# Optimization experiments

Hardware: AMD Instinct MI355X
Metric: run time of the kernel (lower is better)

The kernel has to match this reference:

```python
import jax, jax.numpy as jnp
import numpy as np

N, D, F_NUM = 262144, 128, 64
TEMPERATURE = 0.5
EPS = 1e-8  # torch F.cosine_similarity eps


def setup_inputs() -> dict:
    key = jax.random.key(0)
    k1, k2 = jax.random.split(key)
    embeddings = jax.random.normal(k1, (N, D), dtype=jnp.float32)
    families = jax.random.randint(k2, (N,), 0, F_NUM, dtype=jnp.int32)
    return {"embeddings": embeddings, "families": families}


def reference(embeddings, families):
    T = TEMPERATURE
    n = embeddings.shape[0]
    # Per-family prototype means (segment mean). All F_NUM families are
    # present w.h.p.; guard counts with max(.,1) to avoid div-by-zero.
    ones = jnp.ones((n,), dtype=embeddings.dtype)
    counts = jax.ops.segment_sum(ones, families, num_segments=F_NUM)
    sums = jax.ops.segment_sum(embeddings, families, num_segments=F_NUM)
    protos = sums / jnp.maximum(counts, 1.0)[:, None]  # [F, D]

    # Cosine similarity matrix [N, F], matching torch eps semantics:
    # x.y / max(||x|| * ||y||, eps)
    dots = embeddings @ protos.T                              # [N, F]
    e_norm = jnp.linalg.norm(embeddings, axis=1)              # [N]
    p_norm = jnp.linalg.norm(protos, axis=1)                  # [F]
    sim = dots / jnp.maximum(e_norm[:, None] * p_norm[None, :], EPS)

    pos = jnp.take_along_axis(sim, families[:, None].astype(jnp.int32), axis=1)[:, 0]  # [N]
    # Source quirk: logits already divided by T, then divided by T again
    # inside logsumexp -> effective sim / T^2. The concatenated logits
    # contain pos + all other prototypes = all F prototypes exactly once.
    lse = jax.nn.logsumexp(sim / (T * T), axis=1)             # [N]
    per_sample = -pos / T + lse                               # [N]
    loss = jnp.sum(per_sample) / n
    return loss[None]  # torch returns shape (1,)
```

## Files before the change

### kernel.cpp

```cpp
#include <hip/hip_runtime.h>
#include <math.h>


#define D_DIM 128
#define F_NUM 64
#define ROWS_A 512

typedef __attribute__((ext_vector_type(8))) short short8;
typedef __attribute__((ext_vector_type(4))) float f32x4;

static __device__ __forceinline__ unsigned short f2bf(float x) {
  union { float f; unsigned u; } v; v.f = x;
  unsigned r = v.u + 0x7FFFu + ((v.u >> 16) & 1u);
  return (unsigned short)(r >> 16);
}

__global__ __launch_bounds__(256, 2) void pass_a(
    const float* __restrict__ emb, const int* __restrict__ fam,
    float* __restrict__ psum)
{
  int t = threadIdx.x, w = t >> 6, lane = t & 63;
  int m16 = lane & 15, q = lane >> 4;
  int dimBase = w * 32;

  f32x4 acc[4][2] = {};
  int rb0 = blockIdx.x * ROWS_A;

  #pragma unroll 2
  for (int s = 0; s < ROWS_A / 32; ++s) {
    int rb = rb0 + s * 32;
    const int* fp = fam + rb + q * 8;
    int fj[8];
    #pragma unroll
    for (int j = 0; j < 8; ++j) fj[j] = fp[j];

    const float* eb = emb + (size_t)(rb + q * 8) * D_DIM + dimBase + m16;
    float x0[8], x1[8];
    #pragma unroll
    for (int j = 0; j < 8; ++j) {
      x0[j] = eb[j * D_DIM];
      x1[j] = eb[j * D_DIM + 16];
    }

    short8 af[4];
    #pragma unroll
    for (int ft = 0; ft < 4; ++ft)
      #pragma unroll
      for (int j = 0; j < 8; ++j)
        af[ft][j] = (fj[j] == ft * 16 + m16) ? (short)0x3F80 : (short)0;

    short8 h0, l0, h1, l1;
    #pragma unroll
    for (int j = 0; j < 8; ++j) {
      unsigned b0 = __float_as_uint(x0[j]);
      h0[j] = (short)(b0 >> 16);
      l0[j] = (short)f2bf(x0[j] - __uint_as_float(b0 & 0xFFFF0000u));
      unsigned b1 = __float_as_uint(x1[j]);
      h1[j] = (short)(b1 >> 16);
      l1[j] = (short)f2bf(x1[j] - __uint_as_float(b1 & 0xFFFF0000u));
    }

    #pragma unroll
    for (int ft = 0; ft < 4; ++ft) {
      acc[ft][0] = __builtin_amdgcn_mfma_f32_16x16x32_bf16(af[ft], h0, acc[ft][0], 0, 0, 0);
      acc[ft][0] = __builtin_amdgcn_mfma_f32_16x16x32_bf16(af[ft], l0, acc[ft][0], 0, 0, 0);
      acc[ft][1] = __builtin_amdgcn_mfma_f32_16x16x32_bf16(af[ft], h1, acc[ft][1], 0, 0, 0);
      acc[ft][1] = __builtin_amdgcn_mfma_f32_16x16x32_bf16(af[ft], l1, acc[ft][1], 0, 0, 0);
    }
  }

  float* outp = psum + (size_t)blockIdx.x * (F_NUM * D_DIM) + dimBase + m16;
  #pragma unroll
  for (int ft = 0; ft < 4; ++ft)
    #pragma unroll
    for (int i = 0; i < 4; ++i) {
      int f = ft * 16 + q * 4 + i;
      outp[(size_t)f * D_DIM]      = acc[ft][0][i];
      outp[(size_t)f * D_DIM + 16] = acc[ft][1][i];
    }
}

__global__ __launch_bounds__(256) void pass_b(
    const float* __restrict__ psum, unsigned short* __restrict__ protoB,
    int nPart)
{
  __shared__ float4 sh[256];
  int t = threadIdx.x, f = blockIdx.x;
  int d4 = t & 31, pg = t >> 5;
  const float4* p4 = (const float4*)psum;
  float4 s = make_float4(0.f, 0.f, 0.f, 0.f);
  int per = nPart >> 3;
  #pragma unroll 8
  for (int i = 0; i < per; ++i) {
    float4 a = p4[(size_t)(pg + 8 * i) * (F_NUM * D_DIM / 4) + f * 32 + d4];
    s.x += a.x; s.y += a.y; s.z += a.z; s.w += a.w;
  }
  sh[t] = s;
  __syncthreads();
  if (t < 32) {
    float4 rsum = sh[t];
    #pragma unroll
    for (int g = 1; g < 8; ++g) {
      float4 a = sh[g * 32 + t];
      rsum.x += a.x; rsum.y += a.y; rsum.z += a.z; rsum.w += a.w;
    }
    float n2 = rsum.x * rsum.x + rsum.y * rsum.y +
               rsum.z * rsum.z + rsum.w * rsum.w;
    n2 += __shfl_xor(n2, 1);  n2 += __shfl_xor(n2, 2);  n2 += __shfl_xor(n2, 4);
    n2 += __shfl_xor(n2, 8);  n2 += __shfl_xor(n2, 16);
    float inv = rsqrtf(fmaxf(n2, 1e-24f));
    ushort4 u;
    u.x = f2bf(rsum.x * inv); u.y = f2bf(rsum.y * inv);
    u.z = f2bf(rsum.z * inv); u.w = f2bf(rsum.w * inv);
    ((ushort4*)protoB)[f * 32 + t] = u;
  }
}

__global__ __launch_bounds__(256) void pass_c(
    const float* __restrict__ emb, const int* __restrict__ fam,
    const unsigned short* __restrict__ protoB, float* __restrict__ part)
{
  __shared__ float sWp[4];
  int t = threadIdx.x, w = t >> 6, lane = t & 63;
  int m16 = lane & 15, q = lane >> 4;
  int S0 = blockIdx.x * 128 + w * 32;

  const float4* E4 = (const float4*)emb;
  const short8* P8 = (const short8*)protoB;

  size_t e0 = (size_t)(S0 + m16) * 32 + q * 2;
  size_t e1 = e0 + 16 * 32;
  int pb = m16 * 16 + q;

  f32x4 acc[2][4] = {};
  float s2a = 0.f, s2b = 0.f;

  #pragma unroll
  for (int ks = 0; ks < 4; ++ks) {
    short8 a0 = P8[pb + ks * 4];
    short8 a1 = P8[pb + 256 + ks * 4];
    short8 a2 = P8[pb + 512 + ks * 4];
    short8 a3 = P8[pb + 768 + ks * 4];

    float4 va = E4[e0 + ks * 8], vb = E4[e0 + ks * 8 + 1];
    s2a += va.x * va.x + va.y * va.y + va.z * va.z + va.w * va.w +
           vb.x * vb.x + vb.y * vb.y + vb.z * vb.z + vb.w * vb.w;
    short8 b0;
    b0[0] = (short)f2bf(va.x); b0[1] = (short)f2bf(va.y);
    b0[2] = (short)f2bf(va.z); b0[3] = (short)f2bf(va.w);
    b0[4] = (short)f2bf(vb.x); b0[5] = (short)f2bf(vb.y);
    b0[6] = (short)f2bf(vb.z); b0[7] = (short)f2bf(vb.w);
    acc[0][0] = __builtin_amdgcn_mfma_f32_16x16x32_bf16(a0, b0, acc[0][0], 0, 0, 0);
    acc[0][1] = __builtin_amdgcn_mfma_f32_16x16x32_bf16(a1, b0, acc[0][1], 0, 0, 0);
    acc[0][2] = __builtin_amdgcn_mfma_f32_16x16x32_bf16(a2, b0, acc[0][2], 0, 0, 0);
    acc[0][3] = __builtin_amdgcn_mfma_f32_16x16x32_bf16(a3, b0, acc[0][3], 0, 0, 0);

    float4 vc = E4[e1 + ks * 8], vd = E4[e1 + ks * 8 + 1];
    s2b += vc.x * vc.x + vc.y * vc.y + vc.z * vc.z + vc.w * vc.w +
           vd.x * vd.x + vd.y * vd.y + vd.z * vd.z + vd.w * vd.w;
    short8 b1;
    b1[0] = (short)f2bf(vc.x); b1[1] = (short)f2bf(vc.y);
    b1[2] = (short)f2bf(vc.z); b1[3] = (short)f2bf(vc.w);
    b1[4] = (short)f2bf(vd.x); b1[5] = (short)f2bf(vd.y);
    b1[6] = (short)f2bf(vd.z); b1[7] = (short)f2bf(vd.w);
    acc[1][0] = __builtin_amdgcn_mfma_f32_16x16x32_bf16(a0, b1, acc[1][0], 0, 0, 0);
    acc[1][1] = __builtin_amdgcn_mfma_f32_16x16x32_bf16(a1, b1, acc[1][1], 0, 0, 0);
    acc[1][2] = __builtin_amdgcn_mfma_f32_16x16x32_bf16(a2, b1, acc[1][2], 0, 0, 0);
    acc[1][3] = __builtin_amdgcn_mfma_f32_16x16x32_bf16(a3, b1, acc[1][3], 0, 0, 0);
  }

  s2a += __shfl_xor(s2a, 16); s2a += __shfl_xor(s2a, 32);
  s2b += __shfl_xor(s2b, 16); s2b += __shfl_xor(s2b, 32);
  float rn0 = rsqrtf(fmaxf(s2a, 1e-20f));
  float rn1 = rsqrtf(fmaxf(s2b, 1e-20f));
  int fr0 = fam[S0 + m16], fr1 = fam[S0 + 16 + m16];

  float wp = 0.f;
  {
    int fh = fr0 >> 4, fq = (fr0 >> 2) & 3, fl = fr0 & 3;
    float es = 0.f, ps = 0.f;
    #pragma unroll
    for (int ft = 0; ft < 4; ++ft)
      #pragma unroll
      for (int i = 0; i < 4; ++i) {
        float sim = acc[0][ft][i] * rn0;
        es += __expf(4.f * sim - 4.f);
        ps += (fq == q && fh == ft && fl == i) ? sim : 0.f;
      }
    es += __shfl_xor(es, 16); es += __shfl_xor(es, 32);
    ps += __shfl_xor(ps, 16); ps += __shfl_xor(ps, 32);
    if (q == 0) wp += 4.f + __logf(es) - 2.f * ps;
  }
  {
    int fh = fr1 >> 4, fq = (fr1 >> 2) & 3, fl = fr1 & 3;
    float es = 0.f, ps = 0.f;
    #pragma unroll
    for (int ft = 0; ft < 4; ++ft)
      #pragma unroll
      for (int i = 0; i < 4; ++i) {
        float sim = acc[1][ft][i] * rn1;
        es += __expf(4.f * sim - 4.f);
        ps += (fq == q && fh == ft && fl == i) ? sim : 0.f;
      }
    es += __shfl_xor(es, 16); es += __shfl_xor(es, 32);
    ps += __shfl_xor(ps, 16); ps += __shfl_xor(ps, 32);
    if (q == 0) wp += 4.f + __logf(es) - 2.f * ps;
  }

  wp += __shfl_xor(wp, 1);  wp += __shfl_xor(wp, 2);  wp += __shfl_xor(wp, 4);
  wp += __shfl_xor(wp, 8);  wp += __shfl_xor(wp, 16); wp += __shfl_xor(wp, 32);
  if (lane == 0) sWp[w] = wp;
  __syncthreads();
  if (t == 0) part[blockIdx.x] = sWp[0] + sWp[1] + sWp[2] + sWp[3];
}

__global__ __launch_bounds__(256) void pass_d(
    const float* __restrict__ part, float* __restrict__ out, float invN, int n)
{
  __shared__ float red[4];
  int t = threadIdx.x, w = t >> 6, lane = t & 63;
  float s = 0.f;
  for (int i = t; i < n; i += 256) s += part[i];
  s += __shfl_xor(s, 1);  s += __shfl_xor(s, 2);  s += __shfl_xor(s, 4);
  s += __shfl_xor(s, 8);  s += __shfl_xor(s, 16); s += __shfl_xor(s, 32);
  if (lane == 0) red[w] = s;
  __syncthreads();
  if (t == 0) out[0] = (red[0] + red[1] + red[2] + red[3]) * invN;
}

extern "C" void kernel_launch(void* const* d_in, const int* in_sizes, int n_in,
                              void* d_out, int out_size, void* d_ws, size_t ws_size,
                              hipStream_t stream) {
  const float* emb = (const float*)d_in[0];
  const int* fam = (const int*)d_in[1];
  int N = in_sizes[0] / D_DIM;
  int blocksA = N / ROWS_A;
  int blocksC = N / 128;

  float* ws = (float*)d_ws;
  float* psum = ws;
  size_t off = (size_t)blocksA * (F_NUM * D_DIM);
  unsigned short* protoB = (unsigned short*)(ws + off); off += (F_NUM * D_DIM) / 2;
  float* part = ws + off;

  pass_a<<<blocksA, 256, 0, stream>>>(emb, fam, psum);
  pass_b<<<F_NUM, 256, 0, stream>>>(psum, protoB, blocksA);
  pass_c<<<blocksC, 256, 0, stream>>>(emb, fam, protoB, part);
  pass_d<<<1, 256, 0, stream>>>(part, (float*)d_out, 1.0f / (float)N, blocksC);
}
```

Baseline: 235.2 us.

## Halve pass_a rows, pack bf16 operands, widen pass_b, fuse final reduction via atomics

Halves the rows per pass_a block and raises its occupancy hint. It also builds the bf16 hi/lo split and one-hot operands as packed 32-bit words, with the low part truncated instead of rounded. pass_b now uses 1024 threads to reduce the larger number of partials and zeroes the output. pass_c atomically adds its scaled partial into the output, which removes the pass_d launch. The intent is more parallelism in pass_a, fewer conversion instructions and one fewer launch, at the cost of more partial-sum traffic, a float result order that varies between runs, and slightly lower precision from truncation.

```diff
diff --git a/kernel.cpp b/kernel.cpp
--- a/kernel.cpp
+++ b/kernel.cpp
@@ -4,10 +4,11 @@
 
 #define D_DIM 128
 #define F_NUM 64
-#define ROWS_A 512
+#define ROWS_A 256
 
 typedef __attribute__((ext_vector_type(8))) short short8;
 typedef __attribute__((ext_vector_type(4))) float f32x4;
+typedef union { short8 s; unsigned u[4]; } pack8;
 
 static __device__ __forceinline__ unsigned short f2bf(float x) {
   union { float f; unsigned u; } v; v.f = x;
@@ -15,7 +16,7 @@
   return (unsigned short)(r >> 16);
 }
 
-__global__ __launch_bounds__(256, 2) void pass_a(
+__global__ __launch_bounds__(256, 4) void pass_a(
     const float* __restrict__ emb, const int* __restrict__ fam,
     float* __restrict__ psum)
 {
@@ -42,30 +43,39 @@
       x1[j] = eb[j * D_DIM + 16];
     }
 
-    short8 af[4];
-    #pragma unroll
-    for (int ft = 0; ft < 4; ++ft)
+    pack8 H0, L0, H1, L1;
+    #pragma unroll
+    for (int p = 0; p < 4; ++p) {
+      unsigned a0 = __float_as_uint(x0[2 * p]);
+      unsigned a1 = __float_as_uint(x0[2 * p + 1]);
+      H0.u[p] = (a0 >> 16) | (a1 & 0xFFFF0000u);
+      float la = x0[2 * p]     - __uint_as_float(a0 & 0xFFFF0000u);
+      float lb = x0[2 * p + 1] - __uint_as_float(a1 & 0xFFFF0000u);
+      L0.u[p] = (__float_as_uint(la) >> 16) | (__float_as_uint(lb) & 0xFFFF0000u);
+      unsigned b0 = __float_as_uint(x1[2 * p]);
+      unsigned b1 = __float_as_uint(x1[2 * p + 1]);
+      H1.u[p] = (b0 >> 16) | (b1 & 0xFFFF0000u);
+      float lc = x1[2 * p]     - __uint_as_float(b0 & 0xFFFF0000u);
+      float ld = x1[2 * p + 1] - __uint_as_float(b1 & 0xFFFF0000u);
+      L1.u[p] = (__float_as_uint(lc) >> 16) | (__float_as_uint(ld) & 0xFFFF0000u);
+    }
+
+    pack8 AF[4];
+    #pragma unroll
+    for (int ft = 0; ft < 4; ++ft) {
+      int tgt = ft * 16 + m16;
       #pragma unroll
-      for (int j = 0; j < 8; ++j)
-        af[ft][j] = (fj[j] == ft * 16 + m16) ? (short)0x3F80 : (short)0;
-
-    short8 h0, l0, h1, l1;
-    #pragma unroll
-    for (int j = 0; j < 8; ++j) {
-      unsigned b0 = __float_as_uint(x0[j]);
-      h0[j] = (short)(b0 >> 16);
-      l0[j] = (short)f2bf(x0[j] - __uint_as_float(b0 & 0xFFFF0000u));
-      unsigned b1 = __float_as_uint(x1[j]);
-      h1[j] = (short)(b1 >> 16);
-      l1[j] = (short)f2bf(x1[j] - __uint_as_float(b1 & 0xFFFF0000u));
+      for (int p = 0; p < 4; ++p)
+        AF[ft].u[p] = (fj[2 * p] == tgt ? 0x3F80u : 0u) |
+                      (fj[2 * p + 1] == tgt ? 0x3F800000u : 0u);
     }
 
     #pragma unroll
     for (int ft = 0; ft < 4; ++ft) {
-      acc[ft][0] = __builtin_amdgcn_mfma_f32_16x16x32_bf16(af[ft], h0, acc[ft][0], 0, 0, 0);
-      acc[ft][0] = __builtin_amdgcn_mfma_f32_16x16x32_bf16(af[ft], l0, acc[ft][0], 0, 0, 0);
-      acc[ft][1] = __builtin_amdgcn_mfma_f32_16x16x32_bf16(af[ft], h1, acc[ft][1], 0, 0, 0);
-      acc[ft][1] = __builtin_amdgcn_mfma_f32_16x16x32_bf16(af[ft], l1, acc[ft][1], 0, 0, 0);
+      acc[ft][0] = __builtin_amdgcn_mfma_f32_16x16x32_bf16(AF[ft].s, H0.s, acc[ft][0], 0, 0, 0);
+      acc[ft][0] = __builtin_amdgcn_mfma_f32_16x16x32_bf16(AF[ft].s, L0.s, acc[ft][0], 0, 0, 0);
+      acc[ft][1] = __builtin_amdgcn_mfma_f32_16x16x32_bf16(AF[ft].s, H1.s, acc[ft][1], 0, 0, 0);
+      acc[ft][1] = __builtin_amdgcn_mfma_f32_16x16x32_bf16(AF[ft].s, L1.s, acc[ft][1], 0, 0, 0);
     }
   }
 
@@ -80,19 +90,20 @@
     }
 }
 
-__global__ __launch_bounds__(256) void pass_b(
+__global__ __launch_bounds__(1024) void pass_b(
     const float* __restrict__ psum, unsigned short* __restrict__ protoB,
-    int nPart)
+    float* __restrict__ out, int nPart)
 {
-  __shared__ float4 sh[256];
+  __shared__ float4 sh[1024];
   int t = threadIdx.x, f = blockIdx.x;
+  if (f == 0 && t == 0) out[0] = 0.f;
   int d4 = t & 31, pg = t >> 5;
   const float4* p4 = (const float4*)psum;
   float4 s = make_float4(0.f, 0.f, 0.f, 0.f);
-  int per = nPart >> 3;
+  int per = nPart >> 5;
   #pragma unroll 8
   for (int i = 0; i < per; ++i) {
-    float4 a = p4[(size_t)(pg + 8 * i) * (F_NUM * D_DIM / 4) + f * 32 + d4];
+    float4 a = p4[(size_t)(pg + 32 * i) * (F_NUM * D_DIM / 4) + f * 32 + d4];
     s.x += a.x; s.y += a.y; s.z += a.z; s.w += a.w;
   }
   sh[t] = s;
@@ -100,7 +111,7 @@
   if (t < 32) {
     float4 rsum = sh[t];
     #pragma unroll
-    for (int g = 1; g < 8; ++g) {
+    for (int g = 1; g < 32; ++g) {
       float4 a = sh[g * 32 + t];
       rsum.x += a.x; rsum.y += a.y; rsum.z += a.z; rsum.w += a.w;
     }
@@ -118,7 +129,8 @@
 
 __global__ __launch_bounds__(256) void pass_c(
     const float* __restrict__ emb, const int* __restrict__ fam,
-    const unsigned short* __restrict__ protoB, float* __restrict__ part)
+    const unsigned short* __restrict__ protoB,
+    float* __restrict__ out, float invN)
 {
   __shared__ float sWp[4];
   int t = threadIdx.x, w = t >> 6, lane = t & 63;
@@ -211,21 +223,8 @@
   wp += __shfl_xor(wp, 8);  wp += __shfl_xor(wp, 16); wp += __shfl_xor(wp, 32);
   if (lane == 0) sWp[w] = wp;
   __syncthreads();
-  if (t == 0) part[blockIdx.x] = sWp[0] + sWp[1] + sWp[2] + sWp[3];
-}
-
-__global__ __launch_bounds__(256) void pass_d(
-    const float* __restrict__ part, float* __restrict__ out, float invN, int n)
-{
-  __shared__ float red[4];
-  int t = threadIdx.x, w = t >> 6, lane = t & 63;
-  float s = 0.f;
-  for (int i = t; i < n; i += 256) s += part[i];
-  s += __shfl_xor(s, 1);  s += __shfl_xor(s, 2);  s += __shfl_xor(s, 4);
-  s += __shfl_xor(s, 8);  s += __shfl_xor(s, 16); s += __shfl_xor(s, 32);
-  if (lane == 0) red[w] = s;
-  __syncthreads();
-  if (t == 0) out[0] = (red[0] + red[1] + red[2] + red[3]) * invN;
+  if (t == 0)
+    unsafeAtomicAdd(out, (sWp[0] + sWp[1] + sWp[2] + sWp[3]) * invN);
 }
 
 extern "C" void kernel_launch(void* const* d_in, const int* in_sizes, int n_in,
@@ -240,11 +239,10 @@
   float* ws = (float*)d_ws;
   float* psum = ws;
   size_t off = (size_t)blocksA * (F_NUM * D_DIM);
-  unsigned short* protoB = (unsigned short*)(ws + off); off += (F_NUM * D_DIM) / 2;
-  float* part = ws + off;
+  unsigned short* protoB = (unsigned short*)(ws + off);
 
   pass_a<<<blocksA, 256, 0, stream>>>(emb, fam, psum);
-  pass_b<<<F_NUM, 256, 0, stream>>>(psum, protoB, blocksA);
-  pass_c<<<blocksC, 256, 0, stream>>>(emb, fam, protoB, part);
-  pass_d<<<1, 256, 0, stream>>>(part, (float*)d_out, 1.0f / (float)N, blocksC);
-}
+  pass_b<<<F_NUM, 1024, 0, stream>>>(psum, protoB, (float*)d_out, blocksA);
+  pass_c<<<blocksC, 256, 0, stream>>>(emb, fam, protoB, (float*)d_out,
+                                      1.0f / (float)N);
+}
```

After: 251.5 us. 1.07x slower.
